# Optimization experiments

Measured on AMD Instinct MI355X. Metric: run time of the kernel, lower is better.

The kernel has to match this reference:

```python
import jax, jax.numpy as jnp
import numpy as np
from jax import lax

B, P, DIM, HEADS, K = 2, 4096, 256, 8, 32
DH = DIM // HEADS
SCALE = DH ** -0.5


def setup_inputs() -> dict:
    key = jax.random.key(0)
    ks = jax.random.split(key, 12)
    s = 0.02
    return {
        "xyz": jax.random.uniform(ks[0], (B, P, 3), dtype=jnp.float32),
        "feats": jax.random.normal(ks[1], (B, P, DIM), dtype=jnp.float32),
        "Wq": jax.random.normal(ks[2], (DIM, DIM), dtype=jnp.float32) * s,
        "Wk": jax.random.normal(ks[3], (DIM, DIM), dtype=jnp.float32) * s,
        "Wv": jax.random.normal(ks[4], (DIM, DIM), dtype=jnp.float32) * s,
        "Wp": jax.random.normal(ks[5], (DIM, DIM), dtype=jnp.float32) * s,
        "bp": jnp.zeros((DIM,), jnp.float32),
        "W1": jax.random.normal(ks[6], (DIM, 3), dtype=jnp.float32) * s,
        "b1": jnp.zeros((DIM,), jnp.float32),
        "W2": jax.random.normal(ks[7], (DIM, DIM), dtype=jnp.float32) * s,
        "b2": jnp.zeros((DIM,), jnp.float32),
    }


def _gather(points, idx):
    # points: (B,N,C), idx: (B,M,K) -> (B,M,K,C)
    return jax.vmap(lambda p, i: p[i])(points, idx)


def reference(xyz, feats, Wq, Wk, Wv, Wp, bp, W1, b1, W2, b2):
    b, p, d = feats.shape
    # kNN via squared euclidean distance (same ordering as cdist)
    d2 = jnp.sum((xyz[:, :, None, :] - xyz[:, None, :, :]) ** 2, axis=-1)  # (B,P,P)
    _, idx = lax.top_k(-d2, K)  # (B,P,K) smallest distances

    neigh_xyz = _gather(xyz, idx)                      # (B,P,K,3)
    relpos = neigh_xyz - xyz[:, :, None, :]            # (B,P,K,3)

    q = (feats @ Wq.T).reshape(b, p, HEADS, DH)        # (B,P,H,Dh)
    k_full = feats @ Wk.T                              # (B,P,D)
    v_full = feats @ Wv.T
    k_nei = _gather(k_full, idx).reshape(b, p, K, HEADS, DH)
    v_nei = _gather(v_full, idx).reshape(b, p, K, HEADS, DH)

    # pos MLP: Linear(3,dim) -> ReLU -> Linear(dim,dim)
    h = jax.nn.relu(relpos @ W1.T + b1)
    pos_bias = (h @ W2.T + b2).reshape(b, p, K, HEADS, DH)

    attn = jnp.einsum('bphd,bpkhd->bpkh', q, k_nei + pos_bias) * SCALE
    attn = jax.nn.softmax(attn, axis=2)                # over K neighbors
    out = jnp.einsum('bpkh,bpkhd->bphd', attn, v_nei + pos_bias).reshape(b, p, d)
    return out @ Wp.T + bp
```

## Files before the change

### kernel.cpp

```cpp
#include <hip/hip_runtime.h>
#include <cstddef>

#define PB 4096
static constexpr float SCALE_F = 0.17677669529663687f;

typedef __attribute__((ext_vector_type(8))) short bf16x8;
typedef __attribute__((ext_vector_type(4))) float f32x4;

static __device__ __forceinline__ unsigned short f2bf(float x) {
  unsigned u = __builtin_bit_cast(unsigned, x);
  u += 0x7fffu + ((u >> 16) & 1u);
  return (unsigned short)(u >> 16);
}
static __device__ __forceinline__ float bf2f(unsigned short h) {
  return __builtin_bit_cast(float, (unsigned)h << 16);
}

__global__ __launch_bounds__(64) void knn_kernel(const float* __restrict__ xyz,
                                                 int* __restrict__ idx_out) {
  const int g = blockIdx.x;
  const int b = g >> 12;
  const int p = g & (PB - 1);
  const int lane = threadIdx.x;
  const float* base = xyz + (size_t)b * PB * 3;
  const float qx = base[p * 3 + 0];
  const float qy = base[p * 3 + 1];
  const float qz = base[p * 3 + 2];
  float list_d = 3.4e38f;
  int list_i = -1;
  for (int c = 0; c < PB / 64; ++c) {
    const int j = (c << 6) + lane;
    const float dx = __fsub_rn(qx, base[j * 3 + 0]);
    const float dy = __fsub_rn(qy, base[j * 3 + 1]);
    const float dz = __fsub_rn(qz, base[j * 3 + 2]);
    const float d2 = __fadd_rn(__fadd_rn(__fmul_rn(dx, dx), __fmul_rn(dy, dy)),
                               __fmul_rn(dz, dz));
    float worst = __shfl(list_d, 31);
    unsigned long long mask = __ballot(d2 < worst);
    while (mask) {
      const int l = __ffsll(mask) - 1;
      mask &= mask - 1;
      const float v = __shfl(d2, l);
      worst = __shfl(list_d, 31);
      if (v < worst) {
        const unsigned long long gt = __ballot((lane < 32) && (list_d > v));
        const int pos = __ffsll(gt) - 1;
        const float pd = __shfl_up(list_d, 1);
        const int pi = __shfl_up(list_i, 1);
        if (lane < 32 && lane >= pos) {
          const bool at = (lane == pos);
          list_d = at ? v : pd;
          list_i = at ? ((c << 6) + l) : pi;
        }
      }
    }
  }
  if (lane < 32) idx_out[(size_t)g * 32 + lane] = list_i;
}

__global__ __launch_bounds__(256) void prep_w(
    const float* __restrict__ Wq, const float* __restrict__ Wk,
    const float* __restrict__ Wv, const float* __restrict__ Wp,
    const float* __restrict__ W2,
    unsigned short* __restrict__ whi, unsigned short* __restrict__ wlo,
    unsigned short* __restrict__ w2bf) {
  const int blk = blockIdx.x;
  const int tid = threadIdx.x;
  if (blk < 1024) {
    const int e = blk * 256 + tid;
    const int m = e >> 16;
    const int off = e & 65535;
    const float* src = (m == 0) ? Wq : (m == 1) ? Wk : (m == 2) ? Wv : Wp;
    const float x = src[off];
    const unsigned short hi = f2bf(x);
    whi[e] = hi;
    wlo[e] = f2bf(x - bf2f(hi));
  } else {
    const int off = (blk - 1024) * 256 + tid;
    w2bf[off] = f2bf(W2[off]);
  }
}

__global__ __launch_bounds__(256) void wqu_kernel(
    const float* __restrict__ Wq, const float* __restrict__ W2,
    unsigned short* __restrict__ wqu_t) {
  __shared__ float w2s[32];
  const int hm = blockIdx.x;
  const int h = hm >> 8;
  const int m = hm & 255;
  const int tid = threadIdx.x;
  if (tid < 32) w2s[tid] = W2[(size_t)((h << 5) + tid) * 256 + m];
  __syncthreads();
  float a = 0.f;
#pragma unroll 8
  for (int t = 0; t < 32; ++t)
    a += Wq[(size_t)((h << 5) + t) * 256 + tid] * w2s[t];
  wqu_t[(size_t)hm * 256 + tid] = f2bf(a);
}

__global__ __launch_bounds__(256) void wop_kernel(
    const float* __restrict__ W2, const float* __restrict__ Wp,
    unsigned short* __restrict__ wop_t) {
  __shared__ float wps[32];
  const int blk = blockIdx.x;
  const int j = blk & 255;
  const int h = blk >> 8;
  const int tid = threadIdx.x;
  if (tid < 32) wps[tid] = Wp[(size_t)j * 256 + (h << 5) + tid];
  __syncthreads();
  float a = 0.f;
#pragma unroll 8
  for (int t = 0; t < 32; ++t)
    a += W2[(size_t)((h << 5) + t) * 256 + tid] * wps[t];
  wop_t[(size_t)j * 2048 + (h << 8) + tid] = f2bf(a);
}

__global__ __launch_bounds__(256) void bpp_kernel(
    const float* __restrict__ b2, const float* __restrict__ Wp,
    const float* __restrict__ bp, float* __restrict__ bpp) {
  __shared__ float b2s[256];
  const int tid = threadIdx.x;
  b2s[tid] = b2[tid];
  __syncthreads();
  float a = bp[tid];
  for (int n = 0; n < 256; ++n) a += b2s[n] * Wp[(size_t)tid * 256 + n];
  bpp[tid] = a;
}

static __device__ __forceinline__ void gemm32_core(
    const float* __restrict__ A, const unsigned short* __restrict__ wh,
    const unsigned short* __restrict__ wl, const int r0,
    unsigned short* ah, unsigned short* al, f32x4 acc[2][4]) {
  const int tid = threadIdx.x;
#pragma unroll
  for (int t = 0; t < 8; ++t) {
    const int idx4 = (t << 8) + tid;
    const int row = idx4 >> 6;
    const int c4 = idx4 & 63;
    const float4 v = *(const float4*)(A + (size_t)(r0 + row) * 256 + (c4 << 2));
    const unsigned short h0 = f2bf(v.x), h1 = f2bf(v.y);
    const unsigned short h2 = f2bf(v.z), h3 = f2bf(v.w);
    const unsigned short l0 = f2bf(v.x - bf2f(h0)), l1 = f2bf(v.y - bf2f(h1));
    const unsigned short l2 = f2bf(v.z - bf2f(h2)), l3 = f2bf(v.w - bf2f(h3));
    const int base = (row << 9) + ((c4 << 3) ^ ((row & 7) << 4));
    *(uint2*)((char*)ah + base) =
        make_uint2((unsigned)h0 | ((unsigned)h1 << 16),
                   (unsigned)h2 | ((unsigned)h3 << 16));
    *(uint2*)((char*)al + base) =
        make_uint2((unsigned)l0 | ((unsigned)l1 << 16),
                   (unsigned)l2 | ((unsigned)l3 << 16));
  }
  __syncthreads();
  const int lane = tid & 63;
  const int w = tid >> 6;
  const int il = lane & 15;
  const int q4 = lane >> 4;
#pragma unroll
  for (int mt = 0; mt < 2; ++mt)
#pragma unroll
    for (int nt = 0; nt < 4; ++nt) acc[mt][nt] = (f32x4){0.f, 0.f, 0.f, 0.f};
#pragma unroll 2
  for (int ks = 0; ks < 8; ++ks) {
    bf16x8 bh[4], bl[4], a0[2], a1[2];
#pragma unroll
    for (int nt = 0; nt < 4; ++nt) {
      const int n = (w << 6) + (nt << 4) + il;
      const size_t off = (size_t)n * 256 + (ks << 5) + (q4 << 3);
      bh[nt] = *(const bf16x8*)(wh + off);
      bl[nt] = *(const bf16x8*)(wl + off);
    }
#pragma unroll
    for (int mt = 0; mt < 2; ++mt) {
      const int row = (mt << 4) + il;
      const int byte = (row << 9) + ((((ks << 5) + (q4 << 3)) << 1) ^ ((row & 7) << 4));
      a0[mt] = *(const bf16x8*)((const char*)ah + byte);
      a1[mt] = *(const bf16x8*)((const char*)al + byte);
    }
#pragma unroll
    for (int mt = 0; mt < 2; ++mt)
#pragma unroll
      for (int nt = 0; nt < 4; ++nt) {
        acc[mt][nt] = __builtin_amdgcn_mfma_f32_16x16x32_bf16(a0[mt], bh[nt], acc[mt][nt], 0, 0, 0);
        acc[mt][nt] = __builtin_amdgcn_mfma_f32_16x16x32_bf16(a1[mt], bh[nt], acc[mt][nt], 0, 0, 0);
        acc[mt][nt] = __builtin_amdgcn_mfma_f32_16x16x32_bf16(a0[mt], bl[nt], acc[mt][nt], 0, 0, 0);
      }
  }
}

__global__ __launch_bounds__(256) void qkv_mfma(
    const float* __restrict__ feats,
    const unsigned short* __restrict__ whi, const unsigned short* __restrict__ wlo,
    float* __restrict__ qb, unsigned short* __restrict__ kb16,
    unsigned short* __restrict__ vb16) {
  __shared__ __align__(16) unsigned short ah[32 * 256];
  __shared__ __align__(16) unsigned short al[32 * 256];
  const int bid = blockIdx.x;
  const int sel = bid % 3;
  const int r0 = (bid / 3) << 5;
  const unsigned short* wh = whi + (size_t)sel * 65536;
  const unsigned short* wl = wlo + (size_t)sel * 65536;
  f32x4 acc[2][4];
  gemm32_core(feats, wh, wl, r0, ah, al, acc);
  const int tid = threadIdx.x;
  const int lane = tid & 63;
  const int w = tid >> 6;
  const int il = lane & 15;
  const int q4 = lane >> 4;
#pragma unroll
  for (int mt = 0; mt < 2; ++mt)
#pragma unroll
    for (int nt = 0; nt < 4; ++nt) {
      const int col = (w << 6) + (nt << 4) + il;
#pragma unroll
      for (int r = 0; r < 4; ++r) {
        const size_t e = (size_t)(r0 + (mt << 4) + (q4 << 2) + r) * 256 + col;
        if (sel == 0) qb[e] = acc[mt][nt][r];
        else if (sel == 1) kb16[e] = f2bf(acc[mt][nt][r]);
        else vb16[e] = f2bf(acc[mt][nt][r]);
      }
    }
}

__global__ __launch_bounds__(256) void u_mfma(
    const float* __restrict__ feats, const unsigned short* __restrict__ wqu_t,
    unsigned short* __restrict__ U) {
  __shared__ __align__(16) unsigned short ah[32 * 256];
  const int r0 = blockIdx.x << 5;
  const int cb = blockIdx.y;
  const int tid = threadIdx.x;
#pragma unroll
  for (int t = 0; t < 8; ++t) {
    const int idx4 = (t << 8) + tid;
    const int row = idx4 >> 6;
    const int c4 = idx4 & 63;
    const float4 v = *(const float4*)(feats + (size_t)(r0 + row) * 256 + (c4 << 2));
    const int base = (row << 9) + ((c4 << 3) ^ ((row & 7) << 4));
    *(uint2*)((char*)ah + base) =
        make_uint2((unsigned)f2bf(v.x) | ((unsigned)f2bf(v.y) << 16),
                   (unsigned)f2bf(v.z) | ((unsigned)f2bf(v.w) << 16));
  }
  __syncthreads();
  const unsigned short* wh = wqu_t + (size_t)cb * 65536;
  const int lane = tid & 63;
  const int w = tid >> 6;
  const int il = lane & 15;
  const int q4 = lane >> 4;
  f32x4 acc[2][4];
#pragma unroll
  for (int mt = 0; mt < 2; ++mt)
#pragma unroll
    for (int nt = 0; nt < 4; ++nt) acc[mt][nt] = (f32x4){0.f, 0.f, 0.f, 0.f};
#pragma unroll 2
  for (int ks = 0; ks < 8; ++ks) {
    bf16x8 bh[4], a0[2];
#pragma unroll
    for (int nt = 0; nt < 4; ++nt) {
      const int n = (w << 6) + (nt << 4) + il;
      bh[nt] = *(const bf16x8*)(wh + (size_t)n * 256 + (ks << 5) + (q4 << 3));
    }
#pragma unroll
    for (int mt = 0; mt < 2; ++mt) {
      const int row = (mt << 4) + il;
      const int byte = (row << 9) + ((((ks << 5) + (q4 << 3)) << 1) ^ ((row & 7) << 4));
      a0[mt] = *(const bf16x8*)((const char*)ah + byte);
    }
#pragma unroll
    for (int mt = 0; mt < 2; ++mt)
#pragma unroll
      for (int nt = 0; nt < 4; ++nt)
        acc[mt][nt] = __builtin_amdgcn_mfma_f32_16x16x32_bf16(a0[mt], bh[nt], acc[mt][nt], 0, 0, 0);
  }
#pragma unroll
  for (int mt = 0; mt < 2; ++mt)
#pragma unroll
    for (int nt = 0; nt < 4; ++nt) {
      const int col = (w << 6) + (nt << 4) + il;
#pragma unroll
      for (int r = 0; r < 4; ++r)
        U[(size_t)(r0 + (mt << 4) + (q4 << 2) + r) * 2048 + (cb << 8) + col] =
            f2bf(acc[mt][nt][r]);
    }
}

template <bool FOLD>
__global__ __launch_bounds__(256) void proj_mfma(
    const float* __restrict__ A,
    const unsigned short* __restrict__ whi, const unsigned short* __restrict__ wlo,
    const unsigned short* __restrict__ c16, const unsigned short* __restrict__ wop_t,
    const float* __restrict__ bias, float* __restrict__ C) {
  __shared__ __align__(16) unsigned short ah[32 * 256];
  __shared__ __align__(16) unsigned short al[32 * 256];
  const int r0 = blockIdx.x << 5;
  f32x4 acc[2][4];
  gemm32_core(A, whi, wlo, r0, ah, al, acc);
  const int tid = threadIdx.x;
  const int lane = tid & 63;
  const int w = tid >> 6;
  const int il = lane & 15;
  const int q4 = lane >> 4;
  if (FOLD) {
#pragma unroll 4
    for (int ks2 = 0; ks2 < 64; ++ks2) {
      bf16x8 af[2];
#pragma unroll
      for (int mt = 0; mt < 2; ++mt)
        af[mt] = *(const bf16x8*)(c16 + (size_t)(r0 + (mt << 4) + il) * 2048 +
                                  (ks2 << 5) + (q4 << 3));
#pragma unroll
      for (int nt = 0; nt < 4; ++nt) {
        const int n = (w << 6) + (nt << 4) + il;
        const bf16x8 bf = *(const bf16x8*)(wop_t + (size_t)n * 2048 +
                                           (ks2 << 5) + (q4 << 3));
#pragma unroll
        for (int mt = 0; mt < 2; ++mt)
          acc[mt][nt] = __builtin_amdgcn_mfma_f32_16x16x32_bf16(af[mt], bf, acc[mt][nt], 0, 0, 0);
      }
    }
  }
#pragma unroll
  for (int mt = 0; mt < 2; ++mt)
#pragma unroll
    for (int nt = 0; nt < 4; ++nt) {
      const int col = (w << 6) + (nt << 4) + il;
      const float bv = bias[col];
#pragma unroll
      for (int r = 0; r < 4; ++r)
        C[(size_t)(r0 + (mt << 4) + (q4 << 2) + r) * 256 + col] = acc[mt][nt][r] + bv;
    }
}

__global__ __launch_bounds__(256) void fused_big(
    const float* __restrict__ xyz, const int* __restrict__ nbr_idx,
    const float* __restrict__ qbuf, const unsigned short* __restrict__ kb16,
    const unsigned short* __restrict__ vb16,
    const float* __restrict__ W1, const float* __restrict__ b1,
    const unsigned short* __restrict__ ubuf,
    unsigned short* __restrict__ c16, float* __restrict__ o_pre) {
  __shared__ __align__(16) unsigned short h_km[32 * 256];
  __shared__ __align__(16) char h_mk[256 * 80];
  __shared__ __align__(16) unsigned short u16l[16 * 256];
  __shared__ float sc_part[4][32][9];
  __shared__ float at_lds[32][9];
  __shared__ __align__(16) char at16[16 * 80];
  __shared__ float q_lds[256];
  __shared__ float rel[32][3];
  __shared__ int nbr_s[32];

  const int g = blockIdx.x;
  const int b = g >> 12;
  const int p = g & (PB - 1);
  const int tid = threadIdx.x;

  if (tid < 32) {
    const int j = nbr_idx[(size_t)g * 32 + tid];
    nbr_s[tid] = j;
    const float* xb = xyz + (size_t)b * PB * 3;
    rel[tid][0] = xb[j * 3 + 0] - xb[p * 3 + 0];
    rel[tid][1] = xb[j * 3 + 1] - xb[p * 3 + 1];
    rel[tid][2] = xb[j * 3 + 2] - xb[p * 3 + 2];
  }
  q_lds[tid] = qbuf[(size_t)g * 256 + tid];
  *(uint4*)((char*)u16l + 4096 + tid * 16) = make_uint4(0, 0, 0, 0);
  if (tid < 160) *(unsigned*)(at16 + 640 + tid * 4) = 0;
  __syncthreads();

  {
    const int half = tid >> 7;
    const int c0 = (tid & 127) << 1;
    const int stg = (tid >> 1) & 7;
    const float w00 = W1[c0 * 3 + 0], w01 = W1[c0 * 3 + 1], w02 = W1[c0 * 3 + 2];
    const float w10 = W1[c0 * 3 + 3], w11 = W1[c0 * 3 + 4], w12 = W1[c0 * 3 + 5];
    const float bb0 = b1[c0], bb1 = b1[c0 + 1];
#pragma unroll 4
    for (int rl = 0; rl < 16; ++rl) {
      const int rr = (half << 4) | ((rl + stg) & 15);
      const float rx = rel[rr][0], ry = rel[rr][1], rz = rel[rr][2];
      const float h0 = fmaxf(bb0 + rx * w00 + ry * w01 + rz * w02, 0.f);
      const float h1 = fmaxf(bb1 + rx * w10 + ry * w11 + rz * w12, 0.f);
      const unsigned short bh0 = f2bf(h0), bh1 = f2bf(h1);
      *(unsigned*)((char*)h_km + (rr << 9) + (((unsigned)c0 << 1) ^ ((rr & 7) << 4))) =
          (unsigned)bh0 | ((unsigned)bh1 << 16);
      *(unsigned short*)(h_mk + c0 * 80 + rr * 2) = bh0;
      *(unsigned short*)(h_mk + (c0 + 1) * 80 + rr * 2) = bh1;
    }
  }
  {
    const int h = tid >> 5;
    const int byte = (h << 9) + ((((tid & 31) << 4)) ^ ((h & 7) << 4));
    const uint4 uv = *(const uint4*)(ubuf + (size_t)g * 2048 + tid * 8);
    *(uint4*)((char*)u16l + byte) = uv;
  }
  __syncthreads();

  const int lane = tid & 63;
  const int w = tid >> 6;
  const int il = lane & 15;
  const int q4 = lane >> 4;
  const int kk = tid & 31;
  const int hh = tid >> 5;

  float sqk = 0.f;
  {
    const int j = nbr_s[kk];
    const unsigned short* krow = kb16 + ((size_t)(b << 12) + j) * 256 + (hh << 5);
#pragma unroll
    for (int c4 = 0; c4 < 4; ++c4) {
      const bf16x8 kv = *(const bf16x8*)(krow + (c4 << 3));
#pragma unroll
      for (int jj = 0; jj < 8; ++jj)
        sqk += q_lds[(hh << 5) + (c4 << 3) + jj] * bf2f((unsigned short)kv[jj]);
    }
  }
  {
    f32x4 accp[2];
    accp[0] = (f32x4){0.f, 0.f, 0.f, 0.f};
    accp[1] = (f32x4){0.f, 0.f, 0.f, 0.f};
#pragma unroll
    for (int ksl = 0; ksl < 2; ++ksl) {
      const int m0 = (w << 6) + (ksl << 5) + (q4 << 3);
      const bf16x8 bfr = *(const bf16x8*)((char*)u16l + (il << 9) +
                                          (((unsigned)m0 << 1) ^ ((il & 7) << 4)));
#pragma unroll
      for (int mt = 0; mt < 2; ++mt) {
        const int row = (mt << 4) + il;
        const bf16x8 afr = *(const bf16x8*)((char*)h_km + (row << 9) +
                                            (((unsigned)m0 << 1) ^ ((row & 7) << 4)));
        accp[mt] = __builtin_amdgcn_mfma_f32_16x16x32_bf16(afr, bfr, accp[mt], 0, 0, 0);
      }
    }
    if (il < 8) {
#pragma unroll
      for (int mt = 0; mt < 2; ++mt)
#pragma unroll
        for (int r = 0; r < 4; ++r)
          sc_part[w][(mt << 4) + (q4 << 2) + r][il] = accp[mt][r];
    }
  }
  __syncthreads();

  {
    float s = sqk + sc_part[0][kk][hh] + sc_part[1][kk][hh] +
              sc_part[2][kk][hh] + sc_part[3][kk][hh];
    s *= SCALE_F;
    float mx = s;
#pragma unroll
    for (int off = 16; off; off >>= 1) mx = fmaxf(mx, __shfl_xor(mx, off));
    const float e = __expf(s - mx);
    float ssum = e;
#pragma unroll
    for (int off = 16; off; off >>= 1) ssum += __shfl_xor(ssum, off);
    const float a = e / ssum;
    at_lds[kk][hh] = a;
    *(unsigned short*)(at16 + hh * 80 + kk * 2) = f2bf(a);
  }
  __syncthreads();

  {
    const bf16x8 afr = *(const bf16x8*)(at16 + il * 80 + (q4 << 4));
    const f32x4 zero = (f32x4){0.f, 0.f, 0.f, 0.f};
#pragma unroll
    for (int nt = 0; nt < 4; ++nt) {
      const int m = (w << 6) + (nt << 4) + il;
      const bf16x8 bfr = *(const bf16x8*)(h_mk + m * 80 + (q4 << 4));
      const f32x4 c = __builtin_amdgcn_mfma_f32_16x16x32_bf16(afr, bfr, zero, 0, 0, 0);
      if (q4 < 2) {
#pragma unroll
        for (int r = 0; r < 4; ++r)
          c16[(size_t)g * 2048 + (size_t)((q4 << 2) + r) * 256 + m] = f2bf(c[r]);
      }
    }
  }

  {
    const int n = tid;
    const int h = n >> 5;
    float o = 0.f;
    const size_t vbase = (size_t)(b << 12) * 256 + n;
#pragma unroll 4
    for (int k = 0; k < 32; ++k)
      o += at_lds[k][h] * bf2f(vb16[vbase + (size_t)nbr_s[k] * 256]);
    o_pre[(size_t)g * 256 + n] = o;
  }
}

__global__ __launch_bounds__(256) void fused_small(
    const float* __restrict__ xyz, const int* __restrict__ nbr_idx,
    const float* __restrict__ qbuf, const unsigned short* __restrict__ kb16,
    const unsigned short* __restrict__ vb16,
    const float* __restrict__ W1, const float* __restrict__ b1,
    const unsigned short* __restrict__ w2bf, const float* __restrict__ b2,
    float* __restrict__ o_pre) {
  __shared__ __align__(16) unsigned short h_lds[32 * 256];
  __shared__ float q_lds[256];
  __shared__ float u_lds[8][256];
  __shared__ float c_lds[8][256];
  __shared__ float at_lds[32][8];
  __shared__ float rel[32][3];
  __shared__ int nbr_s[32];

  const int g = blockIdx.x;
  const int b = g >> 12;
  const int p = g & (PB - 1);
  const int tid = threadIdx.x;

  if (tid < 32) {
    const int j = nbr_idx[(size_t)g * 32 + tid];
    nbr_s[tid] = j;
    const float* xb = xyz + (size_t)b * PB * 3;
    rel[tid][0] = xb[j * 3 + 0] - xb[p * 3 + 0];
    rel[tid][1] = xb[j * 3 + 1] - xb[p * 3 + 1];
    rel[tid][2] = xb[j * 3 + 2] - xb[p * 3 + 2];
  }
  q_lds[tid] = qbuf[(size_t)g * 256 + tid];
  __syncthreads();

  {
    const int half = tid >> 7;
    const int c0 = (tid & 127) << 1;
    const float w00 = W1[c0 * 3 + 0], w01 = W1[c0 * 3 + 1], w02 = W1[c0 * 3 + 2];
    const float w10 = W1[c0 * 3 + 3], w11 = W1[c0 * 3 + 4], w12 = W1[c0 * 3 + 5];
    const float bb0 = b1[c0], bb1 = b1[c0 + 1];
#pragma unroll 4
    for (int rl = 0; rl < 16; ++rl) {
      const int rr = (half << 4) + rl;
      const float rx = rel[rr][0], ry = rel[rr][1], rz = rel[rr][2];
      const float h0 = fmaxf(bb0 + rx * w00 + ry * w01 + rz * w02, 0.f);
      const float h1 = fmaxf(bb1 + rx * w10 + ry * w11 + rz * w12, 0.f);
      const unsigned pk = (unsigned)f2bf(h0) | ((unsigned)f2bf(h1) << 16);
      *(unsigned*)((char*)h_lds + (rr << 9) + (((unsigned)c0 << 1) ^ ((rr & 7) << 4))) = pk;
    }
  }
  {
    const int h = tid >> 5;
    const int m8 = (tid & 31) << 3;
    float ua[8];
#pragma unroll
    for (int j = 0; j < 8; ++j) ua[j] = 0.f;
    const unsigned short* wrow = w2bf + (size_t)(h << 5) * 256 + m8;
#pragma unroll 4
    for (int i = 0; i < 32; ++i) {
      const float qn = q_lds[(h << 5) + i];
      const bf16x8 wv = *(const bf16x8*)(wrow + (size_t)i * 256);
#pragma unroll
      for (int j = 0; j < 8; ++j) ua[j] += qn * bf2f((unsigned short)wv[j]);
    }
#pragma unroll
    for (int j = 0; j < 8; ++j) u_lds[h][m8 + j] = ua[j];
  }
  __syncthreads();

  {
    const int k = tid & 31;
    const int h = tid >> 5;
    const int j = nbr_s[k];
    const unsigned short* krow = kb16 + ((size_t)(b << 12) + j) * 256 + (h << 5);
    float s = 0.f;
#pragma unroll
    for (int c4 = 0; c4 < 4; ++c4) {
      const bf16x8 kv = *(const bf16x8*)(krow + (c4 << 3));
#pragma unroll
      for (int jj = 0; jj < 8; ++jj)
        s += q_lds[(h << 5) + (c4 << 3) + jj] * bf2f((unsigned short)kv[jj]);
    }
#pragma unroll 4
    for (int m8 = 0; m8 < 32; ++m8) {
      const bf16x8 hv = *(const bf16x8*)((const char*)h_lds + (k << 9) +
                                         ((m8 << 4) ^ ((k & 7) << 4)));
      const float4 u0 = *(const float4*)&u_lds[h][m8 << 3];
      const float4 u1 = *(const float4*)&u_lds[h][(m8 << 3) + 4];
      s += u0.x * bf2f((unsigned short)hv[0]) + u0.y * bf2f((unsigned short)hv[1]) +
           u0.z * bf2f((unsigned short)hv[2]) + u0.w * bf2f((unsigned short)hv[3]) +
           u1.x * bf2f((unsigned short)hv[4]) + u1.y * bf2f((unsigned short)hv[5]) +
           u1.z * bf2f((unsigned short)hv[6]) + u1.w * bf2f((unsigned short)hv[7]);
    }
    s *= SCALE_F;
    float mx = s;
#pragma unroll
    for (int off = 16; off; off >>= 1) mx = fmaxf(mx, __shfl_xor(mx, off));
    const float e = __expf(s - mx);
    float ssum = e;
#pragma unroll
    for (int off = 16; off; off >>= 1) ssum += __shfl_xor(ssum, off);
    at_lds[k][h] = e / ssum;
  }
  __syncthreads();

  {
    const int m = tid;
    float ca[8];
#pragma unroll
    for (int h = 0; h < 8; ++h) ca[h] = 0.f;
#pragma unroll 4
    for (int k = 0; k < 32; ++k) {
      const float hv = bf2f(*(const unsigned short*)(
          (const char*)h_lds + (k << 9) + ((2 * m) ^ ((k & 7) << 4))));
      const float4 a0 = *(const float4*)&at_lds[k][0];
      const float4 a1 = *(const float4*)&at_lds[k][4];
      ca[0] += a0.x * hv; ca[1] += a0.y * hv; ca[2] += a0.z * hv; ca[3] += a0.w * hv;
      ca[4] += a1.x * hv; ca[5] += a1.y * hv; ca[6] += a1.z * hv; ca[7] += a1.w * hv;
    }
#pragma unroll
    for (int h = 0; h < 8; ++h) c_lds[h][m] = ca[h];
  }
  __syncthreads();

  {
    const int n = tid;
    const int h = n >> 5;
    float o = b2[n];
    const size_t vbase = (size_t)(b << 12) * 256 + n;
#pragma unroll 4
    for (int k = 0; k < 32; ++k)
      o += at_lds[k][h] * bf2f(vb16[vbase + (size_t)nbr_s[k] * 256]);
    const unsigned short* wrow = w2bf + (size_t)n * 256;
    float opos = 0.f;
#pragma unroll 4
    for (int m8 = 0; m8 < 32; ++m8) {
      const bf16x8 wv = *(const bf16x8*)(wrow + (m8 << 3));
      const float4 c0 = *(const float4*)&c_lds[h][m8 << 3];
      const float4 c1 = *(const float4*)&c_lds[h][(m8 << 3) + 4];
      opos += c0.x * bf2f((unsigned short)wv[0]) + c0.y * bf2f((unsigned short)wv[1]) +
              c0.z * bf2f((unsigned short)wv[2]) + c0.w * bf2f((unsigned short)wv[3]) +
              c1.x * bf2f((unsigned short)wv[4]) + c1.y * bf2f((unsigned short)wv[5]) +
              c1.z * bf2f((unsigned short)wv[6]) + c1.w * bf2f((unsigned short)wv[7]);
    }
    o_pre[(size_t)g * 256 + n] = o + opos;
  }
}

extern "C" void kernel_launch(void* const* d_in, const int* in_sizes, int n_in,
                              void* d_out, int out_size, void* d_ws, size_t ws_size,
                              hipStream_t stream) {
  (void)in_sizes; (void)n_in; (void)out_size;
  const float* xyz   = (const float*)d_in[0];
  const float* feats = (const float*)d_in[1];
  const float* Wq    = (const float*)d_in[2];
  const float* Wk    = (const float*)d_in[3];
  const float* Wv    = (const float*)d_in[4];
  const float* Wp    = (const float*)d_in[5];
  const float* bp    = (const float*)d_in[6];
  const float* W1    = (const float*)d_in[7];
  const float* b1    = (const float*)d_in[8];
  const float* W2    = (const float*)d_in[9];
  const float* b2    = (const float*)d_in[10];
  float* out = (float*)d_out;

  float* wsf = (float*)d_ws;
  int* idxw            = (int*)wsf;
  float* qb            = wsf + 262144;
  unsigned short* kb16 = (unsigned short*)(wsf + 2359296);
  unsigned short* vb16 = (unsigned short*)(wsf + 3407872);
  float* op            = wsf + 4456448;
  unsigned short* whi  = (unsigned short*)(wsf + 6553600);
  unsigned short* wlo  = (unsigned short*)(wsf + 6684672);
  unsigned short* w2bf = (unsigned short*)(wsf + 6815744);
  unsigned short* wqut = (unsigned short*)(wsf + 6848512);
  unsigned short* wopt = (unsigned short*)(wsf + 7110656);
  float* bpp           = wsf + 7372800;
  unsigned short* c16  = (unsigned short*)(wsf + 7373056);
  const bool big = ws_size >= (size_t)15761664 * 4;

  hipLaunchKernelGGL(prep_w, dim3(1280), dim3(256), 0, stream,
                     Wq, Wk, Wv, Wp, W2, whi, wlo, w2bf);
  hipLaunchKernelGGL(knn_kernel, dim3(2 * PB), dim3(64), 0, stream, xyz, idxw);
  hipLaunchKernelGGL(qkv_mfma, dim3(768), dim3(256), 0, stream,
                     feats, whi, wlo, qb, kb16, vb16);
  if (big) {
    hipLaunchKernelGGL(wqu_kernel, dim3(2048), dim3(256), 0, stream, Wq, W2, wqut);
    hipLaunchKernelGGL(wop_kernel, dim3(2048), dim3(256), 0, stream, W2, Wp, wopt);
    hipLaunchKernelGGL(bpp_kernel, dim3(1), dim3(256), 0, stream, b2, Wp, bp, bpp);
    hipLaunchKernelGGL(u_mfma, dim3(256, 8), dim3(256), 0, stream,
                       feats, wqut, c16);
    hipLaunchKernelGGL(fused_big, dim3(2 * PB), dim3(256), 0, stream,
                       xyz, idxw, qb, kb16, vb16, W1, b1, c16, c16, op);
    hipLaunchKernelGGL(proj_mfma<true>, dim3(256), dim3(256), 0, stream,
                       op, whi + (size_t)3 * 65536, wlo + (size_t)3 * 65536,
                       c16, wopt, bpp, out);
  } else {
    hipLaunchKernelGGL(fused_small, dim3(2 * PB), dim3(256), 0, stream,
                       xyz, idxw, qb, kb16, vb16, W1, b1, w2bf, b2, op);
    hipLaunchKernelGGL(proj_mfma<false>, dim3(256), dim3(256), 0, stream,
                       op, whi + (size_t)3 * 65536, wlo + (size_t)3 * 65536,
                       nullptr, nullptr, bp, out);
  }
}
```

Measured before the change: 358.0 us.

## Merge weight prep and QKV/U GEMM kernels, stage kNN points in LDS

Folds the wqu, wop and bpp weight-folding kernels into a single prep kernel, and the U GEMM into the QKV GEMM launch, cutting the launch count. The bpp reduction becomes one block per output with a wave-shuffle reduction instead of one serial 256-thread block. The kNN kernel now processes four queries per 256-thread block and stages candidate coordinates in shared memory, so global loads are shared across waves. It also drops a float attention LDS buffer and reads the bf16 copy instead, which costs some precision in the V accumulation and adds block-wide barriers to kNN.

```diff
diff --git a/kernel.cpp b/kernel.cpp
--- a/kernel.cpp
+++ b/kernel.cpp
@@ -16,41 +16,52 @@
   return __builtin_bit_cast(float, (unsigned)h << 16);
 }
 
-__global__ __launch_bounds__(64) void knn_kernel(const float* __restrict__ xyz,
-                                                 int* __restrict__ idx_out) {
-  const int g = blockIdx.x;
+__global__ __launch_bounds__(256) void knn_kernel(const float* __restrict__ xyz,
+                                                  int* __restrict__ idx_out) {
+  __shared__ float xs[768];
+  const int wid = threadIdx.x >> 6;
+  const int lane = threadIdx.x & 63;
+  const int g = (blockIdx.x << 2) + wid;
   const int b = g >> 12;
   const int p = g & (PB - 1);
-  const int lane = threadIdx.x;
   const float* base = xyz + (size_t)b * PB * 3;
   const float qx = base[p * 3 + 0];
   const float qy = base[p * 3 + 1];
   const float qz = base[p * 3 + 2];
   float list_d = 3.4e38f;
   int list_i = -1;
-  for (int c = 0; c < PB / 64; ++c) {
-    const int j = (c << 6) + lane;
-    const float dx = __fsub_rn(qx, base[j * 3 + 0]);
-    const float dy = __fsub_rn(qy, base[j * 3 + 1]);
-    const float dz = __fsub_rn(qz, base[j * 3 + 2]);
-    const float d2 = __fadd_rn(__fadd_rn(__fmul_rn(dx, dx), __fmul_rn(dy, dy)),
-                               __fmul_rn(dz, dz));
-    float worst = __shfl(list_d, 31);
-    unsigned long long mask = __ballot(d2 < worst);
-    while (mask) {
-      const int l = __ffsll(mask) - 1;
-      mask &= mask - 1;
-      const float v = __shfl(d2, l);
-      worst = __shfl(list_d, 31);
-      if (v < worst) {
-        const unsigned long long gt = __ballot((lane < 32) && (list_d > v));
-        const int pos = __ffsll(gt) - 1;
-        const float pd = __shfl_up(list_d, 1);
-        const int pi = __shfl_up(list_i, 1);
-        if (lane < 32 && lane >= pos) {
-          const bool at = (lane == pos);
-          list_d = at ? v : pd;
-          list_i = at ? ((c << 6) + l) : pi;
+  for (int c = 0; c < 16; ++c) {
+    __syncthreads();
+    const int src = c * 768 + threadIdx.x;
+    xs[threadIdx.x]       = base[src];
+    xs[threadIdx.x + 256] = base[src + 256];
+    xs[threadIdx.x + 512] = base[src + 512];
+    __syncthreads();
+#pragma unroll
+    for (int s = 0; s < 4; ++s) {
+      const int jl = (s << 6) + lane;
+      const float dx = __fsub_rn(qx, xs[jl * 3 + 0]);
+      const float dy = __fsub_rn(qy, xs[jl * 3 + 1]);
+      const float dz = __fsub_rn(qz, xs[jl * 3 + 2]);
+      const float d2 = __fadd_rn(__fadd_rn(__fmul_rn(dx, dx), __fmul_rn(dy, dy)),
+                                 __fmul_rn(dz, dz));
+      float worst = __shfl(list_d, 31);
+      unsigned long long mask = __ballot(d2 < worst);
+      while (mask) {
+        const int l = __ffsll(mask) - 1;
+        mask &= mask - 1;
+        const float v = __shfl(d2, l);
+        worst = __shfl(list_d, 31);
+        if (v < worst) {
+          const unsigned long long gt = __ballot((lane < 32) && (list_d > v));
+          const int pos = __ffsll(gt) - 1;
+          const float pd = __shfl_up(list_d, 1);
+          const int pi = __shfl_up(list_i, 1);
+          if (lane < 32 && lane >= pos) {
+            const bool at = (lane == pos);
+            list_d = at ? v : pd;
+            list_i = at ? ((c << 8) + (s << 6) + l) : pi;
+          }
         }
       }
     }
@@ -58,12 +69,15 @@
   if (lane < 32) idx_out[(size_t)g * 32 + lane] = list_i;
 }
 
-__global__ __launch_bounds__(256) void prep_w(
+__global__ __launch_bounds__(256) void prep_all(
     const float* __restrict__ Wq, const float* __restrict__ Wk,
     const float* __restrict__ Wv, const float* __restrict__ Wp,
-    const float* __restrict__ W2,
+    const float* __restrict__ W2, const float* __restrict__ b2,
+    const float* __restrict__ bp,
     unsigned short* __restrict__ whi, unsigned short* __restrict__ wlo,
-    unsigned short* __restrict__ w2bf) {
+    unsigned short* __restrict__ w2bf, unsigned short* __restrict__ wqu_t,
+    unsigned short* __restrict__ wop_t, float* __restrict__ bpp) {
+  __shared__ float sbuf[32];
   const int blk = blockIdx.x;
   const int tid = threadIdx.x;
   if (blk < 1024) {
@@ -75,56 +89,40 @@
     const unsigned short hi = f2bf(x);
     whi[e] = hi;
     wlo[e] = f2bf(x - bf2f(hi));
-  } else {
+  } else if (blk < 1280) {
     const int off = (blk - 1024) * 256 + tid;
     w2bf[off] = f2bf(W2[off]);
-  }
-}
-
-__global__ __launch_bounds__(256) void wqu_kernel(
-    const float* __restrict__ Wq, const float* __restrict__ W2,
-    unsigned short* __restrict__ wqu_t) {
-  __shared__ float w2s[32];
-  const int hm = blockIdx.x;
-  const int h = hm >> 8;
-  const int m = hm & 255;
-  const int tid = threadIdx.x;
-  if (tid < 32) w2s[tid] = W2[(size_t)((h << 5) + tid) * 256 + m];
-  __syncthreads();
-  float a = 0.f;
+  } else if (blk < 3328) {
+    const int hm = blk - 1280;
+    const int h = hm >> 8;
+    const int m = hm & 255;
+    if (tid < 32) sbuf[tid] = W2[(size_t)((h << 5) + tid) * 256 + m];
+    __syncthreads();
+    float a = 0.f;
 #pragma unroll 8
-  for (int t = 0; t < 32; ++t)
-    a += Wq[(size_t)((h << 5) + t) * 256 + tid] * w2s[t];
-  wqu_t[(size_t)hm * 256 + tid] = f2bf(a);
-}
-
-__global__ __launch_bounds__(256) void wop_kernel(
-    const float* __restrict__ W2, const float* __restrict__ Wp,
-    unsigned short* __restrict__ wop_t) {
-  __shared__ float wps[32];
-  const int blk = blockIdx.x;
-  const int j = blk & 255;
-  const int h = blk >> 8;
-  const int tid = threadIdx.x;
-  if (tid < 32) wps[tid] = Wp[(size_t)j * 256 + (h << 5) + tid];
-  __syncthreads();
-  float a = 0.f;
+    for (int t = 0; t < 32; ++t)
+      a += Wq[(size_t)((h << 5) + t) * 256 + tid] * sbuf[t];
+    wqu_t[(size_t)hm * 256 + tid] = f2bf(a);
+  } else if (blk < 5376) {
+    const int e = blk - 3328;
+    const int j = e & 255;
+    const int h = e >> 8;
+    if (tid < 32) sbuf[tid] = Wp[(size_t)j * 256 + (h << 5) + tid];
+    __syncthreads();
+    float a = 0.f;
 #pragma unroll 8
-  for (int t = 0; t < 32; ++t)
-    a += W2[(size_t)((h << 5) + t) * 256 + tid] * wps[t];
-  wop_t[(size_t)j * 2048 + (h << 8) + tid] = f2bf(a);
-}
-
-__global__ __launch_bounds__(256) void bpp_kernel(
-    const float* __restrict__ b2, const float* __restrict__ Wp,
-    const float* __restrict__ bp, float* __restrict__ bpp) {
-  __shared__ float b2s[256];
-  const int tid = threadIdx.x;
-  b2s[tid] = b2[tid];
-  __syncthreads();
-  float a = bp[tid];
-  for (int n = 0; n < 256; ++n) a += b2s[n] * Wp[(size_t)tid * 256 + n];
-  bpp[tid] = a;
+    for (int t = 0; t < 32; ++t)
+      a += W2[(size_t)((h << 5) + t) * 256 + tid] * sbuf[t];
+    wop_t[(size_t)j * 2048 + (h << 8) + tid] = f2bf(a);
+  } else {
+    const int j = blk - 5376;
+    float v = b2[tid] * Wp[(size_t)j * 256 + tid];
+#pragma unroll
+    for (int off = 32; off; off >>= 1) v += __shfl_xor(v, off);
+    if ((tid & 63) == 0) sbuf[tid >> 6] = v;
+    __syncthreads();
+    if (tid == 0) bpp[j] = bp[j] + sbuf[0] + sbuf[1] + sbuf[2] + sbuf[3];
+  }
 }
 
 static __device__ __forceinline__ void gemm32_core(
@@ -187,99 +185,93 @@
   }
 }
 
-__global__ __launch_bounds__(256) void qkv_mfma(
+__global__ __launch_bounds__(256) void qkvu_mfma(
     const float* __restrict__ feats,
     const unsigned short* __restrict__ whi, const unsigned short* __restrict__ wlo,
+    const unsigned short* __restrict__ wqu_t,
     float* __restrict__ qb, unsigned short* __restrict__ kb16,
-    unsigned short* __restrict__ vb16) {
+    unsigned short* __restrict__ vb16, unsigned short* __restrict__ U) {
   __shared__ __align__(16) unsigned short ah[32 * 256];
   __shared__ __align__(16) unsigned short al[32 * 256];
   const int bid = blockIdx.x;
-  const int sel = bid % 3;
-  const int r0 = (bid / 3) << 5;
-  const unsigned short* wh = whi + (size_t)sel * 65536;
-  const unsigned short* wl = wlo + (size_t)sel * 65536;
-  f32x4 acc[2][4];
-  gemm32_core(feats, wh, wl, r0, ah, al, acc);
   const int tid = threadIdx.x;
   const int lane = tid & 63;
   const int w = tid >> 6;
   const int il = lane & 15;
   const int q4 = lane >> 4;
-#pragma unroll
-  for (int mt = 0; mt < 2; ++mt)
-#pragma unroll
-    for (int nt = 0; nt < 4; ++nt) {
-      const int col = (w << 6) + (nt << 4) + il;
-#pragma unroll
-      for (int r = 0; r < 4; ++r) {
-        const size_t e = (size_t)(r0 + (mt << 4) + (q4 << 2) + r) * 256 + col;
-        if (sel == 0) qb[e] = acc[mt][nt][r];
-        else if (sel == 1) kb16[e] = f2bf(acc[mt][nt][r]);
-        else vb16[e] = f2bf(acc[mt][nt][r]);
-      }
-    }
-}
-
-__global__ __launch_bounds__(256) void u_mfma(
-    const float* __restrict__ feats, const unsigned short* __restrict__ wqu_t,
-    unsigned short* __restrict__ U) {
-  __shared__ __align__(16) unsigned short ah[32 * 256];
-  const int r0 = blockIdx.x << 5;
-  const int cb = blockIdx.y;
-  const int tid = threadIdx.x;
-#pragma unroll
-  for (int t = 0; t < 8; ++t) {
-    const int idx4 = (t << 8) + tid;
-    const int row = idx4 >> 6;
-    const int c4 = idx4 & 63;
-    const float4 v = *(const float4*)(feats + (size_t)(r0 + row) * 256 + (c4 << 2));
-    const int base = (row << 9) + ((c4 << 3) ^ ((row & 7) << 4));
-    *(uint2*)((char*)ah + base) =
-        make_uint2((unsigned)f2bf(v.x) | ((unsigned)f2bf(v.y) << 16),
-                   (unsigned)f2bf(v.z) | ((unsigned)f2bf(v.w) << 16));
-  }
-  __syncthreads();
-  const unsigned short* wh = wqu_t + (size_t)cb * 65536;
-  const int lane = tid & 63;
-  const int w = tid >> 6;
-  const int il = lane & 15;
-  const int q4 = lane >> 4;
-  f32x4 acc[2][4];
-#pragma unroll
-  for (int mt = 0; mt < 2; ++mt)
-#pragma unroll
-    for (int nt = 0; nt < 4; ++nt) acc[mt][nt] = (f32x4){0.f, 0.f, 0.f, 0.f};
+  if (bid < 768) {
+    const int sel = bid % 3;
+    const int r0 = (bid / 3) << 5;
+    const unsigned short* wh = whi + (size_t)sel * 65536;
+    const unsigned short* wl = wlo + (size_t)sel * 65536;
+    f32x4 acc[2][4];
+    gemm32_core(feats, wh, wl, r0, ah, al, acc);
+#pragma unroll
+    for (int mt = 0; mt < 2; ++mt)
+#pragma unroll
+      for (int nt = 0; nt < 4; ++nt) {
+        const int col = (w << 6) + (nt << 4) + il;
+#pragma unroll
+        for (int r = 0; r < 4; ++r) {
+          const size_t e = (size_t)(r0 + (mt << 4) + (q4 << 2) + r) * 256 + col;
+          if (sel == 0) qb[e] = acc[mt][nt][r];
+          else if (sel == 1) kb16[e] = f2bf(acc[mt][nt][r]);
+          else vb16[e] = f2bf(acc[mt][nt][r]);
+        }
+      }
+  } else {
+    const int t = bid - 768;
+    const int r0 = (t & 255) << 5;
+    const int cb = t >> 8;
+#pragma unroll
+    for (int tt = 0; tt < 8; ++tt) {
+      const int idx4 = (tt << 8) + tid;
+      const int row = idx4 >> 6;
+      const int c4 = idx4 & 63;
+      const float4 v = *(const float4*)(feats + (size_t)(r0 + row) * 256 + (c4 << 2));
+      const int base = (row << 9) + ((c4 << 3) ^ ((row & 7) << 4));
+      *(uint2*)((char*)ah + base) =
+          make_uint2((unsigned)f2bf(v.x) | ((unsigned)f2bf(v.y) << 16),
+                     (unsigned)f2bf(v.z) | ((unsigned)f2bf(v.w) << 16));
+    }
+    __syncthreads();
+    const unsigned short* wh = wqu_t + (size_t)cb * 65536;
+    f32x4 acc[2][4];
+#pragma unroll
+    for (int mt = 0; mt < 2; ++mt)
+#pragma unroll
+      for (int nt = 0; nt < 4; ++nt) acc[mt][nt] = (f32x4){0.f, 0.f, 0.f, 0.f};
 #pragma unroll 2
-  for (int ks = 0; ks < 8; ++ks) {
-    bf16x8 bh[4], a0[2];
-#pragma unroll
-    for (int nt = 0; nt < 4; ++nt) {
-      const int n = (w << 6) + (nt << 4) + il;
-      bh[nt] = *(const bf16x8*)(wh + (size_t)n * 256 + (ks << 5) + (q4 << 3));
-    }
-#pragma unroll
-    for (int mt = 0; mt < 2; ++mt) {
-      const int row = (mt << 4) + il;
-      const int byte = (row << 9) + ((((ks << 5) + (q4 << 3)) << 1) ^ ((row & 7) << 4));
-      a0[mt] = *(const bf16x8*)((const char*)ah + byte);
+    for (int ks = 0; ks < 8; ++ks) {
+      bf16x8 bh[4], a0[2];
+#pragma unroll
+      for (int nt = 0; nt < 4; ++nt) {
+        const int n = (w << 6) + (nt << 4) + il;
+        bh[nt] = *(const bf16x8*)(wh + (size_t)n * 256 + (ks << 5) + (q4 << 3));
+      }
+#pragma unroll
+      for (int mt = 0; mt < 2; ++mt) {
+        const int row = (mt << 4) + il;
+        const int byte = (row << 9) + ((((ks << 5) + (q4 << 3)) << 1) ^ ((row & 7) << 4));
+        a0[mt] = *(const bf16x8*)((const char*)ah + byte);
+      }
+#pragma unroll
+      for (int mt = 0; mt < 2; ++mt)
+#pragma unroll
+        for (int nt = 0; nt < 4; ++nt)
+          acc[mt][nt] = __builtin_amdgcn_mfma_f32_16x16x32_bf16(a0[mt], bh[nt], acc[mt][nt], 0, 0, 0);
     }
 #pragma unroll
     for (int mt = 0; mt < 2; ++mt)
 #pragma unroll
-      for (int nt = 0; nt < 4; ++nt)
-        acc[mt][nt] = __builtin_amdgcn_mfma_f32_16x16x32_bf16(a0[mt], bh[nt], acc[mt][nt], 0, 0, 0);
-  }
-#pragma unroll
-  for (int mt = 0; mt < 2; ++mt)
-#pragma unroll
-    for (int nt = 0; nt < 4; ++nt) {
-      const int col = (w << 6) + (nt << 4) + il;
-#pragma unroll
-      for (int r = 0; r < 4; ++r)
-        U[(size_t)(r0 + (mt << 4) + (q4 << 2) + r) * 2048 + (cb << 8) + col] =
-            f2bf(acc[mt][nt][r]);
-    }
+      for (int nt = 0; nt < 4; ++nt) {
+        const int col = (w << 6) + (nt << 4) + il;
+#pragma unroll
+        for (int r = 0; r < 4; ++r)
+          U[(size_t)(r0 + (mt << 4) + (q4 << 2) + r) * 2048 + (cb << 8) + col] =
+              f2bf(acc[mt][nt][r]);
+      }
+  }
 }
 
 template <bool FOLD>
@@ -340,7 +332,6 @@
   __shared__ __align__(16) char h_mk[256 * 80];
   __shared__ __align__(16) unsigned short u16l[16 * 256];
   __shared__ float sc_part[4][32][9];
-  __shared__ float at_lds[32][9];
   __shared__ __align__(16) char at16[16 * 80];
   __shared__ float q_lds[256];
   __shared__ float rel[32][3];
@@ -449,9 +440,7 @@
     float ssum = e;
 #pragma unroll
     for (int off = 16; off; off >>= 1) ssum += __shfl_xor(ssum, off);
-    const float a = e / ssum;
-    at_lds[kk][hh] = a;
-    *(unsigned short*)(at16 + hh * 80 + kk * 2) = f2bf(a);
+    *(unsigned short*)(at16 + hh * 80 + kk * 2) = f2bf(e / ssum);
   }
   __syncthreads();
 
@@ -477,8 +466,10 @@
     float o = 0.f;
     const size_t vbase = (size_t)(b << 12) * 256 + n;
 #pragma unroll 4
-    for (int k = 0; k < 32; ++k)
-      o += at_lds[k][h] * bf2f(vb16[vbase + (size_t)nbr_s[k] * 256]);
+    for (int k = 0; k < 32; ++k) {
+      const float aw = bf2f(*(const unsigned short*)(at16 + h * 80 + k * 2));
+      o += aw * bf2f(vb16[vbase + (size_t)nbr_s[k] * 256]);
+    }
     o_pre[(size_t)g * 256 + n] = o;
   }
 }
@@ -660,17 +651,12 @@
   unsigned short* c16  = (unsigned short*)(wsf + 7373056);
   const bool big = ws_size >= (size_t)15761664 * 4;
 
-  hipLaunchKernelGGL(prep_w, dim3(1280), dim3(256), 0, stream,
-                     Wq, Wk, Wv, Wp, W2, whi, wlo, w2bf);
-  hipLaunchKernelGGL(knn_kernel, dim3(2 * PB), dim3(64), 0, stream, xyz, idxw);
-  hipLaunchKernelGGL(qkv_mfma, dim3(768), dim3(256), 0, stream,
-                     feats, whi, wlo, qb, kb16, vb16);
+  hipLaunchKernelGGL(prep_all, dim3(big ? 5632 : 1280), dim3(256), 0, stream,
+                     Wq, Wk, Wv, Wp, W2, b2, bp, whi, wlo, w2bf, wqut, wopt, bpp);
+  hipLaunchKernelGGL(knn_kernel, dim3(2 * PB / 4), dim3(256), 0, stream, xyz, idxw);
+  hipLaunchKernelGGL(qkvu_mfma, dim3(big ? 2816 : 768), dim3(256), 0, stream,
+                     feats, whi, wlo, wqut, qb, kb16, vb16, c16);
   if (big) {
-    hipLaunchKernelGGL(wqu_kernel, dim3(2048), dim3(256), 0, stream, Wq, W2, wqut);
-    hipLaunchKernelGGL(wop_kernel, dim3(2048), dim3(256), 0, stream, W2, Wp, wopt);
-    hipLaunchKernelGGL(bpp_kernel, dim3(1), dim3(256), 0, stream, b2, Wp, bp, bpp);
-    hipLaunchKernelGGL(u_mfma, dim3(256, 8), dim3(256), 0, stream,
-                       feats, wqut, c16);
     hipLaunchKernelGGL(fused_big, dim3(2 * PB), dim3(256), 0, stream,
                        xyz, idxw, qb, kb16, vb16, W1, b1, c16, c16, op);
     hipLaunchKernelGGL(proj_mfma<true>, dim3(256), dim3(256), 0, stream,
```

New measurement: 346.1 us. 3.3% less time.
